# Kernel tuning notes

Measured on AMD Instinct MI355X. Metric: run time of the kernel, lower is better.

The kernel has to match this reference:

```python
import jax, jax.numpy as jnp
import numpy as np

N_NODES = 50000
N_EDGES = 600000
D = 128            # out_feats
N_ETYPES = 4
N_STEPS = 5


def setup_inputs() -> dict:
    key = jax.random.key(0)
    ks = jax.random.split(key, 10)
    h = jax.random.normal(ks[0], (N_NODES, D), dtype=jnp.float32)
    src = jax.random.randint(ks[1], (N_EDGES,), 0, N_NODES)
    dst = jax.random.randint(ks[2], (N_EDGES,), 0, N_NODES)
    # rel_type values are 1..n_etypes in the original module
    etypes = jax.random.randint(ks[3], (N_EDGES,), 1, N_ETYPES + 1)
    s = 1.0 / np.sqrt(D)
    # per-edge-type Linear(out_feats, out_feats): y = x @ W.T + b
    W_lin = jax.random.normal(ks[4], (N_ETYPES, D, D), dtype=jnp.float32) * s
    b_lin = jnp.zeros((N_ETYPES, D), dtype=jnp.float32)
    # GRUCell params (torch layout: rows ordered r, z, n)
    w_ih = jax.random.uniform(ks[5], (3 * D, D), minval=-s, maxval=s, dtype=jnp.float32)
    w_hh = jax.random.uniform(ks[6], (3 * D, D), minval=-s, maxval=s, dtype=jnp.float32)
    b_ih = jax.random.uniform(ks[7], (3 * D,), minval=-s, maxval=s, dtype=jnp.float32)
    b_hh = jax.random.uniform(ks[8], (3 * D,), minval=-s, maxval=s, dtype=jnp.float32)
    return {"h": h, "src": src, "dst": dst, "etypes": etypes,
            "W_lin": W_lin, "b_lin": b_lin,
            "w_ih": w_ih, "w_hh": w_hh, "b_ih": b_ih, "b_hh": b_hh}


def _gru_cell(a, h, w_ih, w_hh, b_ih, b_hh):
    gi = a @ w_ih.T + b_ih          # [N, 3D]
    gh = h @ w_hh.T + b_hh          # [N, 3D]
    i_r, i_z, i_n = jnp.split(gi, 3, axis=-1)
    h_r, h_z, h_n = jnp.split(gh, 3, axis=-1)
    r = jax.nn.sigmoid(i_r + h_r)
    z = jax.nn.sigmoid(i_z + h_z)
    n = jnp.tanh(i_n + r * h_n)
    return (1.0 - z) * n + z * h


def reference(h, src, dst, etypes, W_lin, b_lin, w_ih, w_hh, b_ih, b_hh):
    N = h.shape[0]
    et = etypes - 1                 # 0-based edge type index
    for _ in range(N_STEPS):
        # per-type node transforms: t[k] = h @ W_lin[k].T + b_lin[k]  -> [K, N, D]
        t = jnp.einsum('nd,kfd->knf', h, W_lin) + b_lin[:, None, :]
        msg = t[et, src]            # gather per-edge transformed source feats [E, D]
        a = jax.ops.segment_sum(msg, dst, num_segments=N)  # scatter-sum aggregation
        h = _gru_cell(a, h, w_ih, w_hh, b_ih, b_hh)
    return h
```

## Files before the change

### kernel.cpp

```cpp
#include <hip/hip_runtime.h>
#include <hip/hip_bf16.h>
#include <cstdint>
#include <cstddef>

#define N_NODES 50000
#define N_EDGES 600000
#define DF 128
#define N_ETYPES 4
#define N_STEPS 5
#define SCAN_NB 196
#define GRU_TILES 3125
#define GRU_BLOCKS 256
#define LIN_BLOCKS 256
#define LSTRIDE 130
#define TSTRIDE 136
#define FILL_CHUNKS 2344
#define FILL_RANGE (N_NODES / 8)

typedef _Float16 f16x8 __attribute__((ext_vector_type(8)));
typedef _Float16 f16x4 __attribute__((ext_vector_type(4)));
typedef _Float16 f16x2 __attribute__((ext_vector_type(2)));
typedef float f32x4 __attribute__((ext_vector_type(4)));

__device__ __forceinline__ float sigmoid_fast(float x) {
    return 1.0f / (1.0f + __expf(-x));
}
__device__ __forceinline__ float tanh_fast(float x) {
    return 1.0f - 2.0f / (__expf(2.0f * x) + 1.0f);
}


__global__ __launch_bounds__(256) void k_cvt_w(
    const float* __restrict__ Wl, const float* __restrict__ wih,
    const float* __restrict__ whh, _Float16* __restrict__ Wl_h,
    _Float16* __restrict__ Bc) {
    int i = blockIdx.x * 256 + threadIdx.x;
    if (i < N_ETYPES * DF * DF) Wl_h[i] = (_Float16)Wl[i];
    int row = i >> 8;
    int k = i & 255;
    float v = (k < 128) ? wih[row * 128 + k] : whh[row * 128 + (k - 128)];
    Bc[i] = (_Float16)v;
}

__global__ __launch_bounds__(256) void k_cvt_h(
    const float* __restrict__ h, _Float16* __restrict__ hh, int n4) {
    int i = blockIdx.x * 256 + threadIdx.x;
    if (i < n4) {
        float4 v = ((const float4*)h)[i];
        f16x4 o;
        o.x = (_Float16)v.x; o.y = (_Float16)v.y;
        o.z = (_Float16)v.z; o.w = (_Float16)v.w;
        ((f16x4*)hh)[i] = o;
    }
}

__global__ __launch_bounds__(256) void k_hist(
    const int* __restrict__ dst, int* __restrict__ deg, int E) {
    int i = blockIdx.x * 256 + threadIdx.x;
    if (i < E) atomicAdd(&deg[dst[i]], 1);
}

__global__ __launch_bounds__(256) void k_part(
    const int* __restrict__ deg, int* __restrict__ part, int N) {
    __shared__ int s[256];
    int t = threadIdx.x, i = blockIdx.x * 256 + t;
    s[t] = (i < N) ? deg[i] : 0;
    __syncthreads();
    for (int off = 128; off > 0; off >>= 1) {
        if (t < off) s[t] += s[t + off];
        __syncthreads();
    }
    if (t == 0) part[blockIdx.x] = s[0];
}

__global__ __launch_bounds__(256) void k_scan1(int* __restrict__ part, int nb) {
    __shared__ int s[256];
    int t = threadIdx.x;
    int v = (t < nb) ? part[t] : 0;
    s[t] = v;
    __syncthreads();
    for (int off = 1; off < 256; off <<= 1) {
        int u = (t >= off) ? s[t - off] : 0;
        __syncthreads();
        s[t] += u;
        __syncthreads();
    }
    if (t < nb) part[t] = s[t] - v;
}

__global__ __launch_bounds__(256) void k_row(
    const int* __restrict__ deg, const int* __restrict__ part,
    int* __restrict__ row_start, int* __restrict__ cursor, int N) {
    __shared__ int s[256];
    int t = threadIdx.x, i = blockIdx.x * 256 + t;
    int d = (i < N) ? deg[i] : 0;
    s[t] = d;
    __syncthreads();
    for (int off = 1; off < 256; off <<= 1) {
        int u = (t >= off) ? s[t - off] : 0;
        __syncthreads();
        s[t] += u;
        __syncthreads();
    }
    int rs = part[blockIdx.x] + s[t] - d;
    if (i < N) {
        row_start[i] = rs;
        cursor[i] = rs;
        if (i == N - 1) row_start[N] = rs + d;
    }
}

__global__ __launch_bounds__(256) void k_fill(
    const int* __restrict__ src, const int* __restrict__ dst,
    const int* __restrict__ ety, int* __restrict__ cursor,
    int* __restrict__ csr, int E) {
    const int range = blockIdx.x & 7;
    const int chunk = blockIdx.x >> 3;
    const int e = chunk * 256 + threadIdx.x;
    const int lo = range * FILL_RANGE;
    const int hi = lo + FILL_RANGE;
    if (e < E) {
        int d = dst[e];
        if (d >= lo && d < hi) {
            int slot = atomicAdd(&cursor[d], 1);
            csr[slot] = src[e] | ((ety[e] - 1) << 16);
        }
    }
}


__global__ __launch_bounds__(1024) void k_lin(
    const _Float16* __restrict__ hh, const _Float16* __restrict__ Wl,
    const float* __restrict__ b_lin, _Float16* __restrict__ t_out, int N) {
    __shared__ _Float16 O[2][N_ETYPES * 16 * TSTRIDE];
    __shared__ __align__(16) char Ast[4][4096];
    const int wave = threadIdx.x >> 6, lane = threadIdx.x & 63;
    const int col16 = lane & 15, quad = lane >> 4;
    const int g = wave >> 2;
    const int s = wave & 3;

    f16x8 b[2][4];
#pragma unroll
    for (int ct = 0; ct < 2; ct++) {
        const _Float16* bp = Wl + (size_t)g * DF * DF
                           + (size_t)(s * 32 + ct * 16 + col16) * DF + quad * 8;
#pragma unroll
        for (int kt = 0; kt < 4; kt++) b[ct][kt] = *(const f16x8*)(bp + kt * 32);
    }
    const float bias0 = b_lin[g * DF + s * 32 + col16];
    const float bias1 = b_lin[g * DF + s * 32 + 16 + col16];

    const int olocal = (wave & 3) * 1024 + lane * 16;
    const int oswl = olocal ^ (((olocal >> 8) & 7) << 4);

    const int abase = col16 * 256 + quad * 16;
    const int axor = (col16 & 7) << 4;

    auto STAGE = [&](int iter) {
        if (wave < 4) {
            int tt = blockIdx.x + iter * LIN_BLOCKS;
            if (tt >= GRU_TILES) tt = GRU_TILES - 1;
            const char* gp = (const char*)hh + (size_t)tt * 4096 + oswl;
            char* lp = &Ast[iter & 3][(wave & 3) * 1024];
            __builtin_amdgcn_global_load_lds(
                (const __attribute__((address_space(1))) void*)gp,
                (__attribute__((address_space(3))) void*)lp, 16, 0, 0);
        }
    };

    const int ek = threadIdx.x >> 8;
    const int erow = (threadIdx.x & 255) >> 4;
    const int ec8 = threadIdx.x & 15;

    STAGE(0);
    STAGE(1);
    asm volatile("s_waitcnt vmcnt(1)" ::: "memory");
    __builtin_amdgcn_s_barrier();
    __builtin_amdgcn_sched_barrier(0);

    int it = 0;
    for (int tile = blockIdx.x; tile < GRU_TILES; tile += LIN_BLOCKS, ++it) {
        const int r0 = tile * 16;
        STAGE(it + 2);

        const char* As = (const char*)Ast[it & 3];
        _Float16* Ob = O[it & 1];

        f16x8 A[4];
#pragma unroll
        for (int kt = 0; kt < 4; kt++) {
            int off = (abase + kt * 64) ^ axor;
            A[kt] = *(const f16x8*)(As + off);
        }

        f32x4 acc0 = {0.f, 0.f, 0.f, 0.f}, acc1 = {0.f, 0.f, 0.f, 0.f};
#pragma unroll
        for (int kt = 0; kt < 4; kt++) {
            acc0 = __builtin_amdgcn_mfma_f32_16x16x32_f16(A[kt], b[0][kt], acc0, 0, 0, 0);
            acc1 = __builtin_amdgcn_mfma_f32_16x16x32_f16(A[kt], b[1][kt], acc1, 0, 0, 0);
        }

        _Float16* Og = Ob + g * (16 * TSTRIDE);
#pragma unroll
        for (int i = 0; i < 4; i++) {
            Og[(quad * 4 + i) * TSTRIDE + s * 32 + col16] = (_Float16)(acc0[i] + bias0);
            Og[(quad * 4 + i) * TSTRIDE + s * 32 + 16 + col16] = (_Float16)(acc1[i] + bias1);
        }

        asm volatile("s_waitcnt vmcnt(1) lgkmcnt(0)" ::: "memory");
        __builtin_amdgcn_s_barrier();
        __builtin_amdgcn_sched_barrier(0);

        f16x8 v = *(const f16x8*)&Ob[ek * (16 * TSTRIDE) + erow * TSTRIDE + ec8 * 8];
        *(f16x8*)(t_out + ((size_t)ek * N + (r0 + erow)) * DF + ec8 * 8) = v;
    }
    asm volatile("s_waitcnt vmcnt(0)" ::: "memory");
}

__global__ __launch_bounds__(256) void k_agg(
    const _Float16* __restrict__ t, const int* __restrict__ row_start,
    const int* __restrict__ csr, _Float16* __restrict__ ah, int N) {
    const int wave = threadIdx.x >> 6, lane = threadIdx.x & 63;
    const int g4 = lane >> 4;
    const int c8 = lane & 15;
    const int n = blockIdx.x * 4 + wave;
    const int beg = row_start[n], end = row_start[n + 1];
    float acc[8] = {0.f, 0.f, 0.f, 0.f, 0.f, 0.f, 0.f, 0.f};
    for (int e = beg; e < end; e += 16) {
        int i0 = e + g4, i1 = e + 4 + g4, i2 = e + 8 + g4, i3 = e + 12 + g4;
        float m0 = (i0 < end) ? 1.0f : 0.0f;
        float m1 = (i1 < end) ? 1.0f : 0.0f;
        float m2 = (i2 < end) ? 1.0f : 0.0f;
        float m3 = (i3 < end) ? 1.0f : 0.0f;
        int j0 = (i0 < end) ? i0 : end - 1;
        int j1 = (i1 < end) ? i1 : end - 1;
        int j2 = (i2 < end) ? i2 : end - 1;
        int j3 = (i3 < end) ? i3 : end - 1;
        int p0 = csr[j0], p1 = csr[j1], p2 = csr[j2], p3 = csr[j3];
        f16x8 x0 = *(const f16x8*)(t + ((((size_t)(p0 >> 16)) * N + (p0 & 0xFFFF)) << 7) + c8 * 8);
        f16x8 x1 = *(const f16x8*)(t + ((((size_t)(p1 >> 16)) * N + (p1 & 0xFFFF)) << 7) + c8 * 8);
        f16x8 x2 = *(const f16x8*)(t + ((((size_t)(p2 >> 16)) * N + (p2 & 0xFFFF)) << 7) + c8 * 8);
        f16x8 x3 = *(const f16x8*)(t + ((((size_t)(p3 >> 16)) * N + (p3 & 0xFFFF)) << 7) + c8 * 8);
#pragma unroll
        for (int j = 0; j < 8; j++) acc[j] += m0 * (float)x0[j];
#pragma unroll
        for (int j = 0; j < 8; j++) acc[j] += m1 * (float)x1[j];
#pragma unroll
        for (int j = 0; j < 8; j++) acc[j] += m2 * (float)x2[j];
#pragma unroll
        for (int j = 0; j < 8; j++) acc[j] += m3 * (float)x3[j];
    }
#pragma unroll
    for (int j = 0; j < 8; j++) {
        acc[j] += __shfl_xor(acc[j], 32, 64);
        acc[j] += __shfl_xor(acc[j], 16, 64);
    }
    if (lane < 16) {
        f16x8 o;
#pragma unroll
        for (int j = 0; j < 8; j++) o[j] = (_Float16)acc[j];
        *(f16x8*)(ah + ((size_t)n << 7) + c8 * 8) = o;
    }
}

__global__ __launch_bounds__(768) void k_gru(
    const _Float16* __restrict__ ah, const _Float16* __restrict__ hh,
    const _Float16* __restrict__ Bc, const float* __restrict__ b_ih,
    const float* __restrict__ b_hh, _Float16* __restrict__ hh_next,
    float* __restrict__ out_f32) {
    __shared__ float X[2][4 * 16 * LSTRIDE];
    __shared__ __align__(16) char Ast[4][8192];
    const int wave = threadIdx.x >> 6, lane = threadIdx.x & 63;
    const int col16 = lane & 15, quad = lane >> 4;
    const int g = wave >> 2;
    const int s = wave & 3;

    f16x8 b[2][8];
#pragma unroll
    for (int ct = 0; ct < 2; ct++) {
        const _Float16* bp = Bc + (((size_t)(g * 128 + s * 32 + ct * 16 + col16)) << 8) + quad * 8;
#pragma unroll
        for (int kt = 0; kt < 8; kt++) b[ct][kt] = *(const f16x8*)(bp + kt * 32);
    }

    const int olocal = (wave & 3) * 1024 + lane * 16;
    const int oswl = olocal ^ (((olocal >> 8) & 7) << 4);
    const char* sbase = (wave < 4) ? (const char*)ah : (const char*)hh;

    const int abase = col16 * 256 + quad * 16;
    const int axor = (col16 & 7) << 4;

    auto STAGE = [&](int iter) {
        if (wave < 8) {
            int tt = blockIdx.x + iter * GRU_BLOCKS;
            if (tt >= GRU_TILES) tt = GRU_TILES - 1;
            const char* gp = sbase + (size_t)tt * 4096 + oswl;
            char* lp = &Ast[iter & 3][wave * 1024];
            __builtin_amdgcn_global_load_lds(
                (const __attribute__((address_space(1))) void*)gp,
                (__attribute__((address_space(3))) void*)lp, 16, 0, 0);
        }
    };

    STAGE(0);
    STAGE(1);
    asm volatile("s_waitcnt vmcnt(1)" ::: "memory");
    __builtin_amdgcn_s_barrier();
    __builtin_amdgcn_sched_barrier(0);

    int it = 0;
    for (int tile = blockIdx.x; tile < GRU_TILES; tile += GRU_BLOCKS, ++it) {
        const int r0 = tile * 16;
        STAGE(it + 2);

        const char* As = (const char*)Ast[it & 3];
        float* Xb = X[it & 1];

        f16x8 A[8];
#pragma unroll
        for (int kt = 0; kt < 8; kt++) {
            int off = ((kt & 4) << 10) + abase + (kt & 3) * 64;
            off ^= axor;
            A[kt] = *(const f16x8*)(As + off);
        }

        f32x4 acc[2][2];
#pragma unroll
        for (int u = 0; u < 2; u++)
#pragma unroll
            for (int ct = 0; ct < 2; ct++) acc[u][ct] = (f32x4){0.f, 0.f, 0.f, 0.f};
#pragma unroll
        for (int kt = 0; kt < 8; kt++) {
            const int set = (g == 2 && kt >= 4) ? 1 : 0;
#pragma unroll
            for (int ct = 0; ct < 2; ct++)
                acc[set][ct] = __builtin_amdgcn_mfma_f32_16x16x32_f16(
                    A[kt], b[ct][kt], acc[set][ct], 0, 0, 0);
        }

#pragma unroll
        for (int ct = 0; ct < 2; ct++) {
            const int cbase = s * 32 + ct * 16 + col16;
            if (g < 2) {
#pragma unroll
                for (int i = 0; i < 4; i++)
                    Xb[g * (16 * LSTRIDE) + (quad * 4 + i) * LSTRIDE + cbase] = acc[0][ct][i];
            } else {
#pragma unroll
                for (int i = 0; i < 4; i++) {
                    Xb[2 * (16 * LSTRIDE) + (quad * 4 + i) * LSTRIDE + cbase] = acc[0][ct][i];
                    Xb[3 * (16 * LSTRIDE) + (quad * 4 + i) * LSTRIDE + cbase] = acc[1][ct][i];
                }
            }
        }

        asm volatile("s_waitcnt vmcnt(1) lgkmcnt(0)" ::: "memory");
        __builtin_amdgcn_s_barrier();
        __builtin_amdgcn_sched_barrier(0);

#pragma unroll
        for (int pazz = 0; pazz < 3; pazz++) {
            int e = threadIdx.x + pazz * 768;
            if (e < 2048) {
                int row = e >> 7, col = e & 127;
                float vr = Xb[0 * (16 * LSTRIDE) + row * LSTRIDE + col];
                float vz = Xb[1 * (16 * LSTRIDE) + row * LSTRIDE + col];
                float vin = Xb[2 * (16 * LSTRIDE) + row * LSTRIDE + col];
                float vhn = Xb[3 * (16 * LSTRIDE) + row * LSTRIDE + col];
                float r = sigmoid_fast(vr + b_ih[col] + b_hh[col]);
                float z = sigmoid_fast(vz + b_ih[128 + col] + b_hh[128 + col]);
                float nn = tanh_fast(vin + b_ih[256 + col] + r * (vhn + b_hh[256 + col]));
                int hoff = (4096 + row * 256 + col * 2) ^ ((row & 7) << 4);
                float hprev = (float)*(const _Float16*)(As + hoff);
                float hv = (1.f - z) * nn + z * hprev;
                size_t idx = ((size_t)(r0 + row) << 7) + col;
                hh_next[idx] = (_Float16)hv;
                if (out_f32) out_f32[idx] = hv;
            }
        }
    }
    asm volatile("s_waitcnt vmcnt(0)" ::: "memory");
}


extern "C" void kernel_launch(void* const* d_in, const int* in_sizes, int n_in,
                              void* d_out, int out_size, void* d_ws, size_t ws_size,
                              hipStream_t stream) {
    const float* h0    = (const float*)d_in[0];
    const int*   src   = (const int*)d_in[1];
    const int*   dst   = (const int*)d_in[2];
    const int*   ety   = (const int*)d_in[3];
    const float* W_lin = (const float*)d_in[4];
    const float* b_lin = (const float*)d_in[5];
    const float* w_ih  = (const float*)d_in[6];
    const float* w_hh  = (const float*)d_in[7];
    const float* b_ih  = (const float*)d_in[8];
    const float* b_hh  = (const float*)d_in[9];
    float* hout = (float*)d_out;

    char* p = (char*)d_ws;
    auto alloc = [&](size_t bytes) -> char* {
        char* r = p;
        p += (bytes + 255) & ~(size_t)255;
        return r;
    };
    _Float16* h_a    = (_Float16*)alloc((size_t)N_NODES * DF * 2);
    _Float16* h_b    = (_Float16*)alloc((size_t)N_NODES * DF * 2);
    _Float16* a_half = (_Float16*)alloc((size_t)N_NODES * DF * 2);
    _Float16* t_half = (_Float16*)alloc((size_t)N_ETYPES * N_NODES * DF * 2);
    _Float16* Wl_h   = (_Float16*)alloc((size_t)N_ETYPES * DF * DF * 2);
    _Float16* Bc     = (_Float16*)alloc((size_t)3 * DF * 2 * DF * 2);
    int* deg       = (int*)alloc((size_t)N_NODES * 4);
    int* row_start = (int*)alloc((size_t)(N_NODES + 1) * 4);
    int* cursor    = (int*)alloc((size_t)N_NODES * 4);
    int* csr       = (int*)alloc((size_t)N_EDGES * 4);
    int* part      = (int*)alloc((size_t)SCAN_NB * 4);

    hipMemsetAsync(deg, 0, (size_t)N_NODES * 4, stream);
    k_cvt_w<<<384, 256, 0, stream>>>(W_lin, w_ih, w_hh, Wl_h, Bc);
    k_cvt_h<<<(N_NODES * DF / 4 + 255) / 256, 256, 0, stream>>>(h0, h_a, N_NODES * DF / 4);
    k_hist<<<(N_EDGES + 255) / 256, 256, 0, stream>>>(dst, deg, N_EDGES);
    k_part<<<SCAN_NB, 256, 0, stream>>>(deg, part, N_NODES);
    k_scan1<<<1, 256, 0, stream>>>(part, SCAN_NB);
    k_row<<<SCAN_NB, 256, 0, stream>>>(deg, part, row_start, cursor, N_NODES);
    k_fill<<<FILL_CHUNKS * 8, 256, 0, stream>>>(src, dst, ety, cursor, csr, N_EDGES);

    _Float16* hc = h_a;
    _Float16* hn = h_b;
    for (int s = 0; s < N_STEPS; s++) {
        k_lin<<<LIN_BLOCKS, 1024, 0, stream>>>(hc, Wl_h, b_lin, t_half, N_NODES);
        k_agg<<<N_NODES / 4, 256, 0, stream>>>(t_half, row_start, csr, a_half, N_NODES);
        float* of = (s == N_STEPS - 1) ? hout : nullptr;
        k_gru<<<GRU_BLOCKS, 768, 0, stream>>>(a_half, hc, Bc, b_ih, b_hh, hn, of);
        _Float16* tmp = hc; hc = hn; hn = tmp;
    }
}
```

Before: 534.0 us.

## Restructure GRU kernel so each wave computes all gates for its columns in registers

The GRU kernel moves from 12 waves, which split gate groups and exchanged results through a large fp32 LDS buffer, to 8 waves. Each wave now computes the r, z, input-n and hidden-n accumulators for its own 16 columns and applies the gate nonlinearity straight from registers. This removes the LDS round trip and one barrier phase per tile, and output goes through a small per-wave transpose buffer for vector stores. Separately, the three setup kernels (weight conversion, h conversion, degree histogram) are merged into one launch, which cuts launch overhead. Each wave now does more MFMA work and holds more register weight data.

```diff
diff --git a/kernel.cpp b/kernel.cpp
--- a/kernel.cpp
+++ b/kernel.cpp
@@ -12,14 +12,12 @@
 #define GRU_TILES 3125
 #define GRU_BLOCKS 256
 #define LIN_BLOCKS 256
-#define LSTRIDE 130
 #define TSTRIDE 136
 #define FILL_CHUNKS 2344
 #define FILL_RANGE (N_NODES / 8)
 
 typedef _Float16 f16x8 __attribute__((ext_vector_type(8)));
 typedef _Float16 f16x4 __attribute__((ext_vector_type(4)));
-typedef _Float16 f16x2 __attribute__((ext_vector_type(2)));
 typedef float f32x4 __attribute__((ext_vector_type(4)));
 
 __device__ __forceinline__ float sigmoid_fast(float x) {
@@ -30,34 +28,28 @@
 }
 
 
-__global__ __launch_bounds__(256) void k_cvt_w(
+__global__ __launch_bounds__(256) void k_setup(
     const float* __restrict__ Wl, const float* __restrict__ wih,
-    const float* __restrict__ whh, _Float16* __restrict__ Wl_h,
-    _Float16* __restrict__ Bc) {
+    const float* __restrict__ whh, const float* __restrict__ h,
+    const int* __restrict__ dst,
+    _Float16* __restrict__ Wl_h, _Float16* __restrict__ Bc,
+    _Float16* __restrict__ hh, int* __restrict__ deg) {
     int i = blockIdx.x * 256 + threadIdx.x;
-    if (i < N_ETYPES * DF * DF) Wl_h[i] = (_Float16)Wl[i];
-    int row = i >> 8;
-    int k = i & 255;
-    float v = (k < 128) ? wih[row * 128 + k] : whh[row * 128 + (k - 128)];
-    Bc[i] = (_Float16)v;
-}
-
-__global__ __launch_bounds__(256) void k_cvt_h(
-    const float* __restrict__ h, _Float16* __restrict__ hh, int n4) {
-    int i = blockIdx.x * 256 + threadIdx.x;
-    if (i < n4) {
+    if (i < N_ETYPES * DF * DF * 3 / 2) {
+        if (i < N_ETYPES * DF * DF) Wl_h[i] = (_Float16)Wl[i];
+        int row = i >> 8;
+        int k = i & 255;
+        float v = (k < 128) ? wih[row * 128 + k] : whh[row * 128 + (k - 128)];
+        Bc[i] = (_Float16)v;
+    }
+    if (i < N_NODES * DF / 4) {
         float4 v = ((const float4*)h)[i];
         f16x4 o;
         o.x = (_Float16)v.x; o.y = (_Float16)v.y;
         o.z = (_Float16)v.z; o.w = (_Float16)v.w;
         ((f16x4*)hh)[i] = o;
     }
-}
-
-__global__ __launch_bounds__(256) void k_hist(
-    const int* __restrict__ dst, int* __restrict__ deg, int E) {
-    int i = blockIdx.x * 256 + threadIdx.x;
-    if (i < E) atomicAdd(&deg[dst[i]], 1);
+    if (i < N_EDGES) atomicAdd(&deg[dst[i]], 1);
 }
 
 __global__ __launch_bounds__(256) void k_part(
@@ -152,7 +144,6 @@
 
     const int olocal = (wave & 3) * 1024 + lane * 16;
     const int oswl = olocal ^ (((olocal >> 8) & 7) << 4);
-
     const int abase = col16 * 256 + quad * 16;
     const int axor = (col16 & 7) << 4;
 
@@ -263,43 +254,52 @@
     }
 }
 
-__global__ __launch_bounds__(768) void k_gru(
+__global__ __launch_bounds__(512) void k_gru(
     const _Float16* __restrict__ ah, const _Float16* __restrict__ hh,
     const _Float16* __restrict__ Bc, const float* __restrict__ b_ih,
     const float* __restrict__ b_hh, _Float16* __restrict__ hh_next,
     float* __restrict__ out_f32) {
-    __shared__ float X[2][4 * 16 * LSTRIDE];
     __shared__ __align__(16) char Ast[4][8192];
+    __shared__ _Float16 Tw[8][16][20];
     const int wave = threadIdx.x >> 6, lane = threadIdx.x & 63;
     const int col16 = lane & 15, quad = lane >> 4;
-    const int g = wave >> 2;
-    const int s = wave & 3;
-
-    f16x8 b[2][8];
-#pragma unroll
-    for (int ct = 0; ct < 2; ct++) {
-        const _Float16* bp = Bc + (((size_t)(g * 128 + s * 32 + ct * 16 + col16)) << 8) + quad * 8;
-#pragma unroll
-        for (int kt = 0; kt < 8; kt++) b[ct][kt] = *(const f16x8*)(bp + kt * 32);
-    }
+    const int c = wave * 16 + col16;
+
+    f16x8 br[8], bz[8], bi[4], bh[4];
+    {
+        const _Float16* Br = Bc + ((size_t)c << 8);
+        const _Float16* Bz = Bc + ((size_t)(128 + c) << 8);
+        const _Float16* Bn = Bc + ((size_t)(256 + c) << 8);
+#pragma unroll
+        for (int kt = 0; kt < 8; kt++) {
+            br[kt] = *(const f16x8*)(Br + kt * 32 + quad * 8);
+            bz[kt] = *(const f16x8*)(Bz + kt * 32 + quad * 8);
+        }
+#pragma unroll
+        for (int kt = 0; kt < 4; kt++) {
+            bi[kt] = *(const f16x8*)(Bn + kt * 32 + quad * 8);
+            bh[kt] = *(const f16x8*)(Bn + 128 + kt * 32 + quad * 8);
+        }
+    }
+    const float bir = b_ih[c] + b_hh[c];
+    const float biz = b_ih[128 + c] + b_hh[128 + c];
+    const float bin_ = b_ih[256 + c];
+    const float bhn_ = b_hh[256 + c];
 
     const int olocal = (wave & 3) * 1024 + lane * 16;
     const int oswl = olocal ^ (((olocal >> 8) & 7) << 4);
     const char* sbase = (wave < 4) ? (const char*)ah : (const char*)hh;
-
     const int abase = col16 * 256 + quad * 16;
     const int axor = (col16 & 7) << 4;
 
     auto STAGE = [&](int iter) {
-        if (wave < 8) {
-            int tt = blockIdx.x + iter * GRU_BLOCKS;
-            if (tt >= GRU_TILES) tt = GRU_TILES - 1;
-            const char* gp = sbase + (size_t)tt * 4096 + oswl;
-            char* lp = &Ast[iter & 3][wave * 1024];
-            __builtin_amdgcn_global_load_lds(
-                (const __attribute__((address_space(1))) void*)gp,
-                (__attribute__((address_space(3))) void*)lp, 16, 0, 0);
-        }
+        int tt = blockIdx.x + iter * GRU_BLOCKS;
+        if (tt >= GRU_TILES) tt = GRU_TILES - 1;
+        const char* gp = sbase + (size_t)tt * 4096 + oswl;
+        char* lp = &Ast[iter & 3][wave * 1024];
+        __builtin_amdgcn_global_load_lds(
+            (const __attribute__((address_space(1))) void*)gp,
+            (__attribute__((address_space(3))) void*)lp, 16, 0, 0);
     };
 
     STAGE(0);
@@ -314,7 +314,6 @@
         STAGE(it + 2);
 
         const char* As = (const char*)Ast[it & 3];
-        float* Xb = X[it & 1];
 
         f16x8 A[8];
 #pragma unroll
@@ -324,60 +323,43 @@
             A[kt] = *(const f16x8*)(As + off);
         }
 
-        f32x4 acc[2][2];
-#pragma unroll
-        for (int u = 0; u < 2; u++)
-#pragma unroll
-            for (int ct = 0; ct < 2; ct++) acc[u][ct] = (f32x4){0.f, 0.f, 0.f, 0.f};
+        f32x4 ar = {0.f, 0.f, 0.f, 0.f}, az = {0.f, 0.f, 0.f, 0.f};
+        f32x4 ai = {0.f, 0.f, 0.f, 0.f}, an = {0.f, 0.f, 0.f, 0.f};
 #pragma unroll
         for (int kt = 0; kt < 8; kt++) {
-            const int set = (g == 2 && kt >= 4) ? 1 : 0;
-#pragma unroll
-            for (int ct = 0; ct < 2; ct++)
-                acc[set][ct] = __builtin_amdgcn_mfma_f32_16x16x32_f16(
-                    A[kt], b[ct][kt], acc[set][ct], 0, 0, 0);
-        }
-
-#pragma unroll
-        for (int ct = 0; ct < 2; ct++) {
-            const int cbase = s * 32 + ct * 16 + col16;
-            if (g < 2) {
-#pragma unroll
-                for (int i = 0; i < 4; i++)
-                    Xb[g * (16 * LSTRIDE) + (quad * 4 + i) * LSTRIDE + cbase] = acc[0][ct][i];
+            ar = __builtin_amdgcn_mfma_f32_16x16x32_f16(A[kt], br[kt], ar, 0, 0, 0);
+            az = __builtin_amdgcn_mfma_f32_16x16x32_f16(A[kt], bz[kt], az, 0, 0, 0);
+        }
+#pragma unroll
+        for (int kt = 0; kt < 4; kt++) {
+            ai = __builtin_amdgcn_mfma_f32_16x16x32_f16(A[kt], bi[kt], ai, 0, 0, 0);
+            an = __builtin_amdgcn_mfma_f32_16x16x32_f16(A[4 + kt], bh[kt], an, 0, 0, 0);
+        }
+
+#pragma unroll
+        for (int i = 0; i < 4; i++) {
+            int row = quad * 4 + i;
+            int hoff = (4096 + row * 256 + c * 2) ^ ((row & 7) << 4);
+            float hprev = (float)*(const _Float16*)(As + hoff);
+            float r = sigmoid_fast(ar[i] + bir);
+            float z = sigmoid_fast(az[i] + biz);
+            float nn = tanh_fast(ai[i] + bin_ + r * (an[i] + bhn_));
+            float hv = (1.f - z) * nn + z * hprev;
+            if (out_f32) {
+                out_f32[((size_t)(r0 + row) << 7) + c] = hv;
             } else {
-#pragma unroll
-                for (int i = 0; i < 4; i++) {
-                    Xb[2 * (16 * LSTRIDE) + (quad * 4 + i) * LSTRIDE + cbase] = acc[0][ct][i];
-                    Xb[3 * (16 * LSTRIDE) + (quad * 4 + i) * LSTRIDE + cbase] = acc[1][ct][i];
-                }
+                Tw[wave][row][col16] = (_Float16)hv;
             }
+        }
+        if (!out_f32) {
+            int row = lane >> 2, ch = lane & 3;
+            f16x4 v = *(const f16x4*)&Tw[wave][row][ch * 4];
+            *(f16x4*)(hh_next + ((size_t)(r0 + row) << 7) + wave * 16 + ch * 4) = v;
         }
 
         asm volatile("s_waitcnt vmcnt(1) lgkmcnt(0)" ::: "memory");
         __builtin_amdgcn_s_barrier();
         __builtin_amdgcn_sched_barrier(0);
-
-#pragma unroll
-        for (int pazz = 0; pazz < 3; pazz++) {
-            int e = threadIdx.x + pazz * 768;
-            if (e < 2048) {
-                int row = e >> 7, col = e & 127;
-                float vr = Xb[0 * (16 * LSTRIDE) + row * LSTRIDE + col];
-                float vz = Xb[1 * (16 * LSTRIDE) + row * LSTRIDE + col];
-                float vin = Xb[2 * (16 * LSTRIDE) + row * LSTRIDE + col];
-                float vhn = Xb[3 * (16 * LSTRIDE) + row * LSTRIDE + col];
-                float r = sigmoid_fast(vr + b_ih[col] + b_hh[col]);
-                float z = sigmoid_fast(vz + b_ih[128 + col] + b_hh[128 + col]);
-                float nn = tanh_fast(vin + b_ih[256 + col] + r * (vhn + b_hh[256 + col]));
-                int hoff = (4096 + row * 256 + col * 2) ^ ((row & 7) << 4);
-                float hprev = (float)*(const _Float16*)(As + hoff);
-                float hv = (1.f - z) * nn + z * hprev;
-                size_t idx = ((size_t)(r0 + row) << 7) + col;
-                hh_next[idx] = (_Float16)hv;
-                if (out_f32) out_f32[idx] = hv;
-            }
-        }
     }
     asm volatile("s_waitcnt vmcnt(0)" ::: "memory");
 }
@@ -417,9 +399,8 @@
     int* part      = (int*)alloc((size_t)SCAN_NB * 4);
 
     hipMemsetAsync(deg, 0, (size_t)N_NODES * 4, stream);
-    k_cvt_w<<<384, 256, 0, stream>>>(W_lin, w_ih, w_hh, Wl_h, Bc);
-    k_cvt_h<<<(N_NODES * DF / 4 + 255) / 256, 256, 0, stream>>>(h0, h_a, N_NODES * DF / 4);
-    k_hist<<<(N_EDGES + 255) / 256, 256, 0, stream>>>(dst, deg, N_EDGES);
+    k_setup<<<(N_NODES * DF / 4 + 255) / 256, 256, 0, stream>>>(
+        W_lin, w_ih, w_hh, h0, dst, Wl_h, Bc, h_a, deg);
     k_part<<<SCAN_NB, 256, 0, stream>>>(deg, part, N_NODES);
     k_scan1<<<1, 256, 0, stream>>>(part, SCAN_NB);
     k_row<<<SCAN_NB, 256, 0, stream>>>(deg, part, row_start, cursor, N_NODES);
@@ -431,7 +412,7 @@
         k_lin<<<LIN_BLOCKS, 1024, 0, stream>>>(hc, Wl_h, b_lin, t_half, N_NODES);
         k_agg<<<N_NODES / 4, 256, 0, stream>>>(t_half, row_start, csr, a_half, N_NODES);
         float* of = (s == N_STEPS - 1) ? hout : nullptr;
-        k_gru<<<GRU_BLOCKS, 768, 0, stream>>>(a_half, hc, Bc, b_ih, b_hh, hn, of);
+        k_gru<<<GRU_BLOCKS, 512, 0, stream>>>(a_half, hc, Bc, b_ih, b_hh, hn, of);
         _Float16* tmp = hc; hc = hn; hn = tmp;
     }
 }
```

Result: faster. 522.3 us (-2.2%).
